# Kernel optimization log

Measured on AMD Instinct MI355X. Metric: run time of the kernel, lower is better.

The kernel has to match this reference:

```python
import jax, jax.numpy as jnp
import numpy as np
from jax import lax

B, N, S, P, FIN, FFUT, H, NB, TOPK = 4, 1437, 56, 28, 10, 6, 64, 2, 5


def layer_norm(x, g, b, eps=1e-5):
    m = x.mean(-1, keepdims=True)
    v = ((x - m) ** 2).mean(-1, keepdims=True)
    return (x - m) * lax.rsqrt(v + eps) * g + b


def conv1d_same(x, w, pl, pr):
    # x: [BNF, 1, S], w: [1, 1, k]; torch Conv1d is cross-correlation == XLA conv
    return lax.conv_general_dilated(x, w, (1,), [(pl, pr)], dimension_numbers=('NCH', 'OIH', 'NCH'))


def gelu(x):
    return jax.nn.gelu(x, approximate=False)


def mixer_block(x, adj, wk, mk, lcg, lcb, ltg, ltb, lfg, lfb, lsg, lsb, tw, tb, fw, fb, sw, sb):
    Bx, Nx, Sx, Fx = x.shape
    # conv branch (pre-norm)
    xn = layer_norm(x, lcg, lcb)
    xc = xn.transpose(0, 1, 3, 2).reshape(Bx * Nx * Fx, 1, Sx)
    weekly = conv1d_same(xc, wk, 3, 3).reshape(Bx, Nx, Fx, Sx).transpose(0, 1, 3, 2)
    monthly = conv1d_same(xc, mk, 13, 14).reshape(Bx, Nx, Fx, Sx).transpose(0, 1, 3, 2)
    x = x + weekly + monthly
    # temporal MLP over S
    xn = layer_norm(x, ltg, ltb)
    xt = gelu(jnp.einsum('bnfs,os->bnfo', xn.transpose(0, 1, 3, 2), tw) + tb)
    x = x + xt.transpose(0, 1, 3, 2)
    # feature MLP over Feat
    xn = layer_norm(x, lfg, lfb)
    x = x + gelu(jnp.einsum('bnsf,of->bnso', xn, fw) + fb)
    # spatial propagation via dense bmm with adj
    xn = layer_norm(x, lsg, lsb)
    xp = jnp.einsum('bnsf,of->bnso', xn, sw).reshape(Bx, Nx, Sx * Fx)
    xs = jnp.einsum('bmn,bnd->bmd', adj, xp).reshape(Bx, Nx, Sx, Fx) + sb
    return x + xs


def reference(x, x_future, adj, fp_w, fp_b, in_ln_g, in_ln_b, q_w, q_b, k_w, k_b,
              node_emb, graph_alpha, blk_weekly, blk_monthly,
              blk_lnc_g, blk_lnc_b, blk_lnt_g, blk_lnt_b, blk_lnf_g, blk_lnf_b,
              blk_lns_g, blk_lns_b, blk_temp_w, blk_temp_b, blk_feat_w, blk_feat_b,
              blk_spat_w, blk_spat_b, futr_w, futr_b, head_w, head_b):
    Bx, Nx, Sx, _ = x.shape
    h = jnp.einsum('bnsf,hf->bnsh', x, fp_w) + fp_b
    h = layer_norm(h, in_ln_g, in_ln_b)
    emb = node_emb / jnp.maximum(jnp.linalg.norm(node_emb, axis=-1, keepdims=True), 1e-12)
    h = h + emb[None, :, None, :]
    # recency-weighted context
    decay = jnp.exp(-jnp.arange(Sx, 0, -1, dtype=jnp.float32) / 14.0)
    rw = decay / decay.sum()
    ctx = (h * rw[None, None, :, None]).sum(2)  # [B,N,H]
    Q = ctx @ q_w.T + q_b
    K = ctx @ k_w.T + k_b
    da = jnp.einsum('bnh,bmh->bnm', Q, K) / jnp.sqrt(jnp.float32(Q.shape[-1]))
    da = jax.nn.relu(jnp.clip(da, -10.0, 10.0))
    _, ti = lax.top_k(da, TOPK)
    mask = jax.vmap(jax.vmap(lambda row, idx: row.at[idx].set(1.0)))(
        jnp.zeros((Bx, Nx, Nx), da.dtype), ti)
    dyn = jax.nn.softmax(jnp.where(mask > 0, da, -jnp.inf), axis=2)
    dyn = jnp.nan_to_num(dyn)
    alpha = jax.nn.sigmoid(graph_alpha)  # shape (1,), broadcasts
    comb = alpha * adj[None, :, :] + (1.0 - alpha) * dyn
    comb = comb / jnp.maximum(jnp.abs(comb).sum(axis=2, keepdims=True), 1e-12)
    for i in range(NB):
        h = mixer_block(h, comb, blk_weekly[i], blk_monthly[i],
                        blk_lnc_g[i], blk_lnc_b[i], blk_lnt_g[i], blk_lnt_b[i],
                        blk_lnf_g[i], blk_lnf_b[i], blk_lns_g[i], blk_lns_b[i],
                        blk_temp_w[i], blk_temp_b[i], blk_feat_w[i], blk_feat_b[i],
                        blk_spat_w[i], blk_spat_b[i])
    hist = h.reshape(Bx, Nx, -1)
    fut = (jnp.einsum('bnpf,hf->bnph', x_future, futr_w) + futr_b).reshape(Bx, Nx, -1)
    feats = jnp.concatenate([hist, fut], axis=2)
    return feats @ head_w.T + head_b


def setup_inputs() -> dict:
    key = jax.random.key(0)
    ks = jax.random.split(key, 16)
    rn = lambda k, shp, s=1.0: jax.random.normal(k, shp, dtype=jnp.float32) * s
    return {
        'x': rn(ks[0], (B, N, S, FIN)),
        'x_future': rn(ks[1], (B, N, P, FFUT)),
        'adj': jax.random.uniform(ks[2], (N, N), dtype=jnp.float32),
        'fp_w': rn(ks[3], (H, FIN), 0.1), 'fp_b': jnp.zeros((H,), jnp.float32),
        'in_ln_g': jnp.ones((H,), jnp.float32), 'in_ln_b': jnp.zeros((H,), jnp.float32),
        'q_w': rn(ks[4], (H, H), 0.1), 'q_b': jnp.zeros((H,), jnp.float32),
        'k_w': rn(ks[5], (H, H), 0.1), 'k_b': jnp.zeros((H,), jnp.float32),
        'node_emb': rn(ks[6], (N, H), 0.02),
        'graph_alpha': jnp.full((1,), 2.2, jnp.float32),
        'blk_weekly': rn(ks[7], (NB, 1, 1, 7), 0.1),
        'blk_monthly': rn(ks[8], (NB, 1, 1, 28), 0.1),
        'blk_lnc_g': jnp.ones((NB, H), jnp.float32), 'blk_lnc_b': jnp.zeros((NB, H), jnp.float32),
        'blk_lnt_g': jnp.ones((NB, H), jnp.float32), 'blk_lnt_b': jnp.zeros((NB, H), jnp.float32),
        'blk_lnf_g': jnp.ones((NB, H), jnp.float32), 'blk_lnf_b': jnp.zeros((NB, H), jnp.float32),
        'blk_lns_g': jnp.ones((NB, H), jnp.float32), 'blk_lns_b': jnp.zeros((NB, H), jnp.float32),
        'blk_temp_w': rn(ks[9], (NB, S, S), 0.1), 'blk_temp_b': jnp.zeros((NB, S), jnp.float32),
        'blk_feat_w': rn(ks[10], (NB, H, H), 0.1), 'blk_feat_b': jnp.zeros((NB, H), jnp.float32),
        'blk_spat_w': rn(ks[11], (NB, H, H), 0.1), 'blk_spat_b': jnp.zeros((NB, H), jnp.float32),
        'futr_w': rn(ks[12], (H, FFUT), 0.1), 'futr_b': jnp.zeros((H,), jnp.float32),
        'head_w': rn(ks[13], (P, S * H + P * H), 0.02), 'head_b': jnp.zeros((P,), jnp.float32),
    }
```

## Files before the change

### kernel.cpp

```cpp
#include <hip/hip_runtime.h>
#include <hip/hip_bf16.h>
#include <math.h>

#define BB 4
#define NN 1437
#define SS 56
#define PP 28
#define FIN 10
#define FFUT 6
#define HH 64
#define NBLK 2
#define TOPK 5
#define DD (SS*HH)
#define FD (PP*HH)
#define TOT (DD+FD)
#define MP 1536
#define KP 1472
#define NT (KP/32)
#define SP 1536
#define WIMG_SZ 16384

typedef __attribute__((ext_vector_type(8))) __bf16 bf16x8;
typedef __attribute__((ext_vector_type(4))) float  f32x4;


__device__ __forceinline__ float gelu_fast(float x){
    float x2 = x*x;
    float u  = __builtin_fmaf(0.044715f*x2, x, x);
    float e  = __builtin_amdgcn_exp2f(2.3022077f*u);
    float r  = __builtin_amdgcn_rcpf(e+1.f);
    return x - x*r;
}
template<int C>
__device__ __forceinline__ float dppadd(float v){
    int x = __builtin_amdgcn_mov_dpp(__float_as_int(v), C, 0xF, 0xF, true);
    return v + __int_as_float(x);
}
__device__ __forceinline__ float row16_sum(float v){
    v = dppadd<0xB1>(v);
    v = dppadd<0x4E>(v);
    v = dppadd<0x141>(v);
    v = dppadd<0x140>(v);
    return v;
}
__device__ __forceinline__ float wave_sum64(float v){
    v = row16_sum(v);
    v += __shfl_xor(v,16,64);
    v += __shfl_xor(v,32,64);
    return v;
}
__device__ __forceinline__ void async_load16(const void* g, void* l){
    __builtin_amdgcn_global_load_lds(
        (const __attribute__((address_space(1))) void*)g,
        (__attribute__((address_space(3))) void*)l, 16, 0, 0);
}
__device__ __forceinline__ unsigned short f2bf(float x){
    unsigned int u = __float_as_uint(x);
    unsigned int r = (u + 0x7fffu + ((u>>16)&1u)) >> 16;
    return (unsigned short)r;
}
__device__ __forceinline__ float bf2f(unsigned short u){
    return __uint_as_float(((unsigned int)u)<<16);
}
__device__ __forceinline__ unsigned long long umax64(unsigned long long a, unsigned long long b){return a>b?a:b;}
__device__ __forceinline__ unsigned long long umin64(unsigned long long a, unsigned long long b){return a<b?a:b;}

__global__ __launch_bounds__(256) void k_front(
    const float* __restrict__ x, const float* __restrict__ fpw, const float* __restrict__ fpb,
    const float* __restrict__ lng, const float* __restrict__ lnb,
    const float* __restrict__ nemb,
    const float* __restrict__ qw, const float* __restrict__ qb,
    const float* __restrict__ kw, const float* __restrict__ kb,
    float* __restrict__ h,
    unsigned short* __restrict__ qpack, unsigned short* __restrict__ kpack)
{
    int bn = blockIdx.x; int n = bn % NN;
    int tid=threadIdx.x; int lane=tid&63; int wv=tid>>6;
    __shared__ float xin[SS*FIN];
    __shared__ float wlds[HH*FIN];
    __shared__ float rw[SS];
    __shared__ float rsum;
    __shared__ float red[4][HH];
    __shared__ float ctxs[HH];
    for (int i=tid;i<SS*FIN;i+=256) xin[i]=x[(size_t)bn*SS*FIN+i];
    for (int i=tid;i<HH*FIN;i+=256) wlds[i]=fpw[i];
    if (tid<SS) rw[tid]=expf(-(float)(SS-tid)/14.0f);
    __syncthreads();
    if (tid==0){ float s=0.f; for(int i=0;i<SS;++i) s+=rw[i]; rsum=s; }
    __syncthreads();
    float inv_rs = 1.0f/rsum;
    float ev = nemb[(size_t)n*HH+lane];
    float ss = wave_sum64(ev*ev);
    float el = ev / fmaxf(sqrtf(ss), 1e-12f);
    float gg=lng[lane], bv=lnb[lane], fb0=fpb[lane];
    int paddr = (lane&15)*4 + (lane>>4);
    float cacc=0.f;
    for (int s=wv;s<SS;s+=4){
        float v=fb0;
        #pragma unroll
        for (int c=0;c<FIN;++c) v += xin[s*FIN+c]*wlds[lane*FIN+c];
        float m = wave_sum64(v)*(1.f/HH);
        float d = v-m;
        float va = wave_sum64(d*d)*(1.f/HH);
        float hn = d*rsqrtf(va+1e-5f)*gg + bv + el;
        h[((size_t)bn*SS+s)*HH + paddr]=hn;
        cacc += hn * rw[s]*inv_rs;
    }
    red[wv][lane]=cacc;
    __syncthreads();
    if (wv==0) ctxs[lane]=red[0][lane]+red[1][lane]+red[2][lane]+red[3][lane];
    __syncthreads();
    if (wv==0){
        const float4* qr = reinterpret_cast<const float4*>(qw + (size_t)lane*HH);
        const float4* kr = reinterpret_cast<const float4*>(kw + (size_t)lane*HH);
        float q=qb[lane], k=kb[lane];
        #pragma unroll 4
        for (int t=0;t<16;++t){
            float4 qv=qr[t], kv=kr[t];
            float c0=ctxs[4*t], c1=ctxs[4*t+1], c2=ctxs[4*t+2], c3=ctxs[4*t+3];
            q += qv.x*c0+qv.y*c1+qv.z*c2+qv.w*c3;
            k += kv.x*c0+kv.y*c1+kv.z*c2+kv.w*c3;
        }
        int b = bn/NN, m = bn%NN;
        size_t off = (size_t)b*8*MP*8 + (size_t)(lane>>3)*MP*8 + (size_t)m*8 + (lane&7);
        qpack[off]=f2bf(q); kpack[off]=f2bf(k);
    }
}

__global__ __launch_bounds__(256) void k_qkt(
    const unsigned short* __restrict__ qp, const unsigned short* __restrict__ kp,
    float* __restrict__ scores)
{
    int bm=blockIdx.x, bnn=blockIdx.y, b=blockIdx.z;
    int tid=threadIdx.x, lane=tid&63, wv=tid>>6;
    int g=lane>>4, c15=lane&15;
    int m0=bm*128, n0=bnn*128;
    __shared__ unsigned short As[8192];
    __shared__ unsigned short Bs[8192];
    const char* qbase = (const char*)(qp + (size_t)b*8*MP*8);
    const char* kbase = (const char*)(kp + (size_t)b*8*MP*8);
    #pragma unroll
    for (int i=0;i<4;++i){
        int idx=i*256+tid; int ch=idx>>7, r=idx&127;
        async_load16(qbase + ((size_t)(ch*MP + m0 + r))*16, (char*)As + idx*16);
        async_load16(kbase + ((size_t)(ch*MP + n0 + r))*16, (char*)Bs + idx*16);
    }
    asm volatile("s_waitcnt vmcnt(0)");
    __syncthreads();
    int wr=wv>>1, wc=wv&1;
    f32x4 acc[4][4];
    #pragma unroll
    for (int i=0;i<4;++i)
        #pragma unroll
        for (int j=0;j<4;++j) acc[i][j]=(f32x4){0.f,0.f,0.f,0.f};
    #pragma unroll
    for (int kc=0;kc<2;++kc){
        bf16x8 af[4], bfv[4];
        #pragma unroll
        for (int i=0;i<4;++i)
            af[i]=*(const bf16x8*)((const char*)As + ((4*kc+g)*128 + wr*64+i*16+c15)*16);
        #pragma unroll
        for (int j=0;j<4;++j)
            bfv[j]=*(const bf16x8*)((const char*)Bs + ((4*kc+g)*128 + wc*64+j*16+c15)*16);
        #pragma unroll
        for (int i=0;i<4;++i)
            #pragma unroll
            for (int j=0;j<4;++j)
                acc[i][j]=__builtin_amdgcn_mfma_f32_16x16x32_bf16(af[i],bfv[j],acc[i][j],0,0,0);
    }
    #pragma unroll
    for (int i=0;i<4;++i){
        #pragma unroll
        for (int q=0;q<4;++q){
            int m = m0 + wr*64 + i*16 + g*4 + q;
            float* sr = scores + ((size_t)b*SP + m)*SP + n0 + wc*64 + c15;
            #pragma unroll
            for (int j=0;j<4;++j){
                float v = acc[i][j][q]*0.125f;
                v = fminf(fmaxf(v,0.f),10.f);
                sr[j*16]=v;
            }
        }
    }
}

#define INS(x) do{ unsigned long long t_=(x); \
    unsigned long long n0_=umax64(u0,t_), t1_=umin64(u0,t_); \
    unsigned long long n1_=umax64(u1,t1_), t2_=umin64(u1,t1_); \
    unsigned long long n2_=umax64(u2,t2_), t3_=umin64(u2,t2_); \
    unsigned long long n3_=umax64(u3,t3_), t4_=umin64(u3,t3_); \
    unsigned long long n4_=umax64(u4,t4_); \
    u0=n0_;u1=n1_;u2=n2_;u3=n3_;u4=n4_; }while(0)

#define MERGE(b0,b1,b2,b3,b4) do{ \
    unsigned long long o0_=umax64(u0,(b0)); \
    unsigned long long o1_=umax64(umax64((b1),umin64(u0,(b0))),u1); \
    unsigned long long o2_=umax64(umax64((b2),umin64(u0,(b1))),umax64(umin64(u1,(b0)),u2)); \
    unsigned long long o3_=umax64(umax64((b3),umin64(u0,(b2))),umax64(umin64(u1,(b1)),umax64(umin64(u2,(b0)),u3))); \
    unsigned long long o4_=umax64(umax64((b4),umin64(u0,(b3))),umax64(umax64(umin64(u1,(b2)),umin64(u2,(b1))),umax64(umin64(u3,(b0)),u4))); \
    u0=o0_;u1=o1_;u2=o2_;u3=o3_;u4=o4_; }while(0)

__global__ __launch_bounds__(256) void k_topk(
    const float* __restrict__ scores, const float* __restrict__ adj,
    const float* __restrict__ galpha, __hip_bfloat16* __restrict__ combh)
{
    int m=blockIdx.x, b=blockIdx.y, tid=threadIdx.x, lane=tid&63, wv=tid>>6;
    __shared__ float row[KP];
    __shared__ unsigned long long wtop[4][8];
    __shared__ float redp[4];
    const float* srow = scores + ((size_t)b*SP + m)*SP;
    unsigned long long u0=0,u1=0,u2=0,u3=0,u4=0;
    for (int n=tid;n<NN;n+=256){
        float v=srow[n];
        unsigned long long key=((unsigned long long)__float_as_uint(v)<<32)|(unsigned long long)(0xFFFFFFFFu-(unsigned)n);
        INS(key);
    }
    #pragma unroll
    for (int off=1; off<64; off<<=1){
        unsigned long long b0=__shfl_xor(u0,off,64), b1=__shfl_xor(u1,off,64),
                           b2=__shfl_xor(u2,off,64), b3=__shfl_xor(u3,off,64),
                           b4=__shfl_xor(u4,off,64);
        MERGE(b0,b1,b2,b3,b4);
    }
    if (lane==0){ wtop[wv][0]=u0; wtop[wv][1]=u1; wtop[wv][2]=u2; wtop[wv][3]=u3; wtop[wv][4]=u4; }
    __syncthreads();
    u0=wtop[0][0]; u1=wtop[0][1]; u2=wtop[0][2]; u3=wtop[0][3]; u4=wtop[0][4];
    #pragma unroll
    for (int w2=1;w2<4;++w2)
        MERGE(wtop[w2][0],wtop[w2][1],wtop[w2][2],wtop[w2][3],wtop[w2][4]);

    float s0=__uint_as_float((unsigned)(u0>>32)), s1=__uint_as_float((unsigned)(u1>>32)),
          s2=__uint_as_float((unsigned)(u2>>32)), s3=__uint_as_float((unsigned)(u3>>32)),
          s4=__uint_as_float((unsigned)(u4>>32));
    int i0=(int)(0xFFFFFFFFu-(unsigned)u0), i1=(int)(0xFFFFFFFFu-(unsigned)u1),
        i2=(int)(0xFFFFFFFFu-(unsigned)u2), i3=(int)(0xFFFFFFFFu-(unsigned)u3),
        i4=(int)(0xFFFFFFFFu-(unsigned)u4);
    float e0=1.f, e1=expf(s1-s0), e2=expf(s2-s0), e3=expf(s3-s0), e4=expf(s4-s0);
    float den=e0+e1+e2+e3+e4;
    float alpha=1.f/(1.f+expf(-galpha[0]));
    float oma=(1.f-alpha)/den;
    float p0=oma*e0, p1=oma*e1, p2=oma*e2, p3=oma*e3, p4=oma*e4;

    const float* arow = adj + (size_t)m*NN;
    float part=0.f;
    for (int n=tid;n<NN;n+=256){
        float v=alpha*arow[n];
        v += (n==i0)?p0:0.f;
        v += (n==i1)?p1:0.f;
        v += (n==i2)?p2:0.f;
        v += (n==i3)?p3:0.f;
        v += (n==i4)?p4:0.f;
        row[n]=v;
        part+=fabsf(v);
    }
    part=wave_sum64(part);
    if (lane==0) redp[wv]=part;
    __syncthreads();
    float inv=1.f/fmaxf(redp[0]+redp[1]+redp[2]+redp[3],1e-12f);
    __hip_bfloat16* dst = combh + ((size_t)b*MP+m)*KP;
    for (int n=tid;n<KP;n+=256){
        float v = (n<NN) ? row[n]*inv : 0.f;
        dst[n]=__float2bfloat16(v);
    }
}
#undef INS
#undef MERGE

__global__ __launch_bounds__(256) void k_prepw(
    const float* __restrict__ wk, const float* __restrict__ mk,
    const float* __restrict__ tw, const float* __restrict__ fw,
    const float* __restrict__ sw, unsigned short* __restrict__ wimg)
{
    int i = blockIdx.x; int tid = threadIdx.x;
    const float* wki = wk + i*7;
    const float* mki = mk + i*28;
    const float* twi = tw + i*SS*SS;
    const float* fwi = fw + i*HH*HH;
    const float* swi = sw + i*HH*HH;
    unsigned short* o = wimg + (size_t)i*WIMG_SZ;
    for (int e=tid; e<4096; e+=256){
        int r = e>>6, k = e&63;
        int swz = ((k*2) ^ ((r&7)<<4)) >> 1;
        float mv = 0.f;
        if (r<SS && k<SS){
            int a = k-r+3;  if (a>=0 && a<7)  mv += wki[a];
            int b2= k-r+13; if (b2>=0 && b2<28) mv += mki[b2];
        }
        o[r*64 + swz] = f2bf(mv);
        float tv = (r<SS && k<SS) ? twi[r*SS+k] : 0.f;
        o[4096 + r*64 + swz] = f2bf(tv);
        int pk = (k>>3)*512 + r*8 + (k&7);
        o[8192  + pk] = f2bf(fwi[r*HH+k]);
        o[12288 + pk] = f2bf(swi[r*HH+k]);
    }
}

__global__ __launch_bounds__(256) void k_prep_head(
    const float* __restrict__ hw, __hip_bfloat16* __restrict__ hw16)
{
    int i = blockIdx.x*256 + threadIdx.x;
    int r = i / TOT, k = i - r*TOT;
    float v = (r<PP) ? hw[(size_t)r*TOT + k] : 0.f;
    hw16[i] = __float2bfloat16(v);
}

__global__ __launch_bounds__(256) void k_fut(
    const float* __restrict__ xf, const float* __restrict__ fw,
    const float* __restrict__ fbias, __hip_bfloat16* __restrict__ feats)
{
    int bn=blockIdx.x, tid=threadIdx.x;
    __shared__ float fwl[HH*FFUT];
    __shared__ float fbl[HH];
    __shared__ float xfl[PP*FFUT];
    for (int i=tid;i<HH*FFUT;i+=256) fwl[i]=fw[i];
    if (tid<HH) fbl[tid]=fbias[tid];
    for (int i=tid;i<PP*FFUT;i+=256) xfl[i]=xf[(size_t)bn*PP*FFUT+i];
    __syncthreads();
    __hip_bfloat16* dst = feats + (size_t)bn*TOT + DD;
    for (int q=tid;q<FD;q+=256){
        int pp=q>>6, hh2=q&63;
        float v=fbl[hh2];
        #pragma unroll
        for (int c2=0;c2<FFUT;++c2) v += xfl[pp*FFUT+c2]*fwl[hh2*FFUT+c2];
        dst[q]=__float2bfloat16(v);
    }
}

__global__ __launch_bounds__(256) void k_mixer2(
    float* __restrict__ h, unsigned short* __restrict__ xpg,
    const unsigned short* __restrict__ spat_in,
    const unsigned short* __restrict__ wimg,
    const float* __restrict__ lncg, const float* __restrict__ lncb,
    const float* __restrict__ lntg, const float* __restrict__ lntb,
    const float* __restrict__ lnfg, const float* __restrict__ lnfb,
    const float* __restrict__ lnsg, const float* __restrict__ lnsb,
    const float* __restrict__ tb, const float* __restrict__ fb)
{
    int bid = blockIdx.x;
    int xx = bid & 7, ii = bid >> 3;
    int bn = (xx < 4) ? xx*719 + ii : 2876 + (xx-4)*718 + ii;
    int tid=threadIdx.x, lane=tid&63, w=tid>>6;
    int g=lane>>4, c=lane&15;
    __shared__ unsigned short wbuf[2][4096];
    __shared__ unsigned short xs[4096];
    __shared__ float prm[640];

    const char* wsrc=(const char*)wimg;
#define LOADW(SLOTB, BUFP) do{ \
    async_load16(wsrc+(size_t)(SLOTB)+((size_t)tid)*16,       (char*)(BUFP)+(w*64)*16); \
    async_load16(wsrc+(size_t)(SLOTB)+((size_t)(256+tid))*16, (char*)(BUFP)+((256+w*64))*16); } while(0)

    LOADW(0,    wbuf[0]);
    LOADW(8192, wbuf[1]);
    if (tid<64){
        prm[tid]      =lncg[tid]; prm[64+tid] =lncb[tid];
        prm[128+tid]  =lntg[tid]; prm[192+tid]=lntb[tid];
        prm[256+tid]  =lnfg[tid]; prm[320+tid]=lnfb[tid];
        prm[384+tid]  =lnsg[tid]; prm[448+tid]=lnsb[tid];
        prm[512+tid]  =(tid<SS)?tb[tid]:0.f;
        prm[576+tid]  =fb[tid];
    }
    float xl[4][4];
    float* hb = h + (size_t)bn*DD;
    int srow = 16*w + 4*g;
    #pragma unroll
    for (int q=0;q<4;++q){
        int s=srow+q;
        if (s<SS){
            const float4 v4 = *reinterpret_cast<const float4*>(hb + s*HH + c*4);
            float a0=v4.x, a1=v4.y, a2=v4.z, a3=v4.w;
            if (spat_in){
                ushort4 sv = *reinterpret_cast<const ushort4*>(spat_in + (size_t)bn*TOT + s*HH + c*4);
                a0 += bf2f(sv.x); a1 += bf2f(sv.y); a2 += bf2f(sv.z); a3 += bf2f(sv.w);
            }
            xl[q][0]=a0; xl[q][1]=a1; xl[q][2]=a2; xl[q][3]=a3;
        } else {
            xl[q][0]=0.f; xl[q][1]=0.f; xl[q][2]=0.f; xl[q][3]=0.f;
        }
    }
    __syncthreads();

    float xn[4][4];
    f32x4 acc[4];

#define LNSTAGE(GOFF,BOFF) do{ \
    _Pragma("unroll") \
    for (int q=0;q<4;++q){ \
        float sv = xl[q][0]+xl[q][1]+xl[q][2]+xl[q][3]; \
        float s2 = xl[q][0]*xl[q][0]+xl[q][1]*xl[q][1]+xl[q][2]*xl[q][2]+xl[q][3]*xl[q][3]; \
        sv = row16_sum(sv); \
        s2 = row16_sum(s2); \
        float mn = sv*(1.f/64.f); \
        float var = s2*(1.f/64.f)-mn*mn; \
        float rstd = rsqrtf(var+1e-5f); \
        bool ok = (srow+q)<SS; \
        _Pragma("unroll") \
        for (int tj=0;tj<4;++tj){ \
            float v=(xl[q][tj]-mn)*rstd*prm[(GOFF)+tj*16+c]+prm[(BOFF)+tj*16+c]; \
            xn[q][tj]= ok ? v : 0.f; \
        } \
    } }while(0)

#define WRITE_XNP() do{ \
    _Pragma("unroll") \
    for (int qp=0;qp<2;++qp){ \
        int s0=srow+2*qp; \
        _Pragma("unroll") \
        for (int tj=0;tj<4;++tj){ \
            unsigned int pv=(unsigned int)f2bf(xn[2*qp][tj])|((unsigned int)f2bf(xn[2*qp+1][tj])<<16); \
            *(unsigned int*)((char*)xs + ((s0>>3)*1024 + (tj*16+c)*16 + (s0&7)*2)) = pv; \
        } \
    } }while(0)

#define WRITE_XNR() do{ \
    _Pragma("unroll") \
    for (int q=0;q<4;++q){ int s=srow+q; \
        _Pragma("unroll") \
        for (int tj=0;tj<4;++tj){ \
            *(unsigned short*)((char*)xs + s*128 + (((tj*16+c)*2) ^ ((s&7)<<4))) = f2bf(xn[q][tj]); \
        } \
    } }while(0)

#define MM(APTR,BPTR) do{ \
    _Pragma("unroll") \
    for (int tj=0;tj<4;++tj) acc[tj]=(f32x4){0.f,0.f,0.f,0.f}; \
    _Pragma("unroll") \
    for (int kc=0;kc<2;++kc){ \
        int arow=16*w+c; \
        bf16x8 af=*(const bf16x8*)((const char*)(APTR)+arow*128+((kc*64+g*16)^((arow&7)<<4))); \
        _Pragma("unroll") \
        for (int tj=0;tj<4;++tj){ \
            bf16x8 bf2=*(const bf16x8*)((const char*)(BPTR)+(kc*4+g)*1024+(tj*16+c)*16); \
            acc[tj]=__builtin_amdgcn_mfma_f32_16x16x32_bf16(af,bf2,acc[tj],0,0,0); \
        } \
    } }while(0)

    LNSTAGE(0,64); WRITE_XNP();
    __syncthreads();
    MM(&wbuf[0][0], xs);
    #pragma unroll
    for (int q=0;q<4;++q)
        #pragma unroll
        for (int tj=0;tj<4;++tj) xl[q][tj]+=acc[tj][q];
    __syncthreads();
    LOADW(16384, wbuf[0]);
    LNSTAGE(128,192); WRITE_XNP();
    __syncthreads();
    MM(&wbuf[1][0], xs);
    #pragma unroll
    for (int q=0;q<4;++q){
        float tbv=prm[512+srow+q];
        #pragma unroll
        for (int tj=0;tj<4;++tj) xl[q][tj]+=gelu_fast(acc[tj][q]+tbv);
    }
    __syncthreads();
    LOADW(24576, wbuf[1]);
    LNSTAGE(256,320); WRITE_XNR();
    __syncthreads();
    MM(xs, &wbuf[0][0]);
    #pragma unroll
    for (int q=0;q<4;++q)
        #pragma unroll
        for (int tj=0;tj<4;++tj) xl[q][tj]+=gelu_fast(acc[tj][q]+prm[576+tj*16+c]);
    __syncthreads();
    LNSTAGE(384,448); WRITE_XNR();
    __syncthreads();
    MM(xs, &wbuf[1][0]);
    int b_=bn/NN, n_=bn%NN;
    unsigned short* xpo = xpg + ((size_t)b_*(KP/8) + (size_t)(n_>>3))*(size_t)DD*8 + (n_&7);
    #pragma unroll
    for (int q=0;q<4;++q){
        int s=srow+q;
        if (s<SS){
            float4 hv; hv.x=xl[q][0]; hv.y=xl[q][1]; hv.z=xl[q][2]; hv.w=xl[q][3];
            *reinterpret_cast<float4*>(hb + s*HH + c*4) = hv;
            #pragma unroll
            for (int tj=0;tj<4;++tj){
                int d = s*HH + tj*16 + c;
                xpo[(size_t)d*8] = f2bf(acc[tj][q]);
            }
        }
    }
#undef LNSTAGE
#undef WRITE_XNP
#undef WRITE_XNR
#undef MM
#undef LOADW
}

__global__ __launch_bounds__(256,4) void k_bmm_mfma(
    const __hip_bfloat16* __restrict__ combh,
    const __hip_bfloat16* __restrict__ xpg,
    const float* __restrict__ sb,
    const float* __restrict__ h,
    unsigned short* __restrict__ spat_out,
    __hip_bfloat16* __restrict__ feats_out)
{
    __shared__ short As[3][2048];
    __shared__ short Bs[3][4096];

    int bid = blockIdx.x;
    int wg = (bid & 7)*336 + (bid >> 3);
    int bm = wg % 24; int tmp2 = wg / 24; int bd = tmp2 % 28; int b = tmp2 / 28;
    int tid=threadIdx.x, lane=tid&63, w=tid>>6;
    int g=lane>>4, c=lane&15;
    int wr=w>>1, wc=w&1;
    int m0=bm*64, d0=bd*128;

    const char* cb = (const char*)(combh + (size_t)b*MP*KP);
    const char* xb = (const char*)(xpg   + (size_t)b*(KP/8)*(size_t)DD*8);

    int arow_s = tid>>2, aslot = tid&3;
    int ag = aslot ^ ((arow_s>>1)&3);
    const char* srcA = cb + ((size_t)(m0+arow_s)*KP + ag*8)*2;
    int bch = tid>>7, bcol = tid&127;
    const char* srcB0 = xb + ((size_t)bch*DD + d0 + bcol)*16;
    const char* srcB1 = xb + ((size_t)(bch+2)*DD + d0 + bcol)*16;
    const size_t BSTEP = (size_t)4*DD*16;

    f32x4 acc[2][4];
    #pragma unroll
    for (int i=0;i<2;++i)
        #pragma unroll
        for (int j=0;j<4;++j) acc[i][j]=(f32x4){0.f,0.f,0.f,0.f};

    int aoff[2], boff[4];
    #pragma unroll
    for (int i=0;i<2;++i){
        int row = 32*wr + 16*i + c;
        aoff[i] = row*64 + ((g*16) ^ (((row>>1)&3)<<4));
    }
    #pragma unroll
    for (int j=0;j<4;++j) boff[j] = (g*128 + 64*wc + 16*j + c)*16;

#define STAGE(BUF,T) do { \
    async_load16(srcA  + (size_t)(T)*64,    (char*)As[BUF] + w*1024); \
    async_load16(srcB0 + (size_t)(T)*BSTEP, (char*)Bs[BUF] + w*1024); \
    async_load16(srcB1 + (size_t)(T)*BSTEP, (char*)Bs[BUF] + 4096 + w*1024); } while(0)

    STAGE(0,0); STAGE(1,1);
    asm volatile("s_waitcnt vmcnt(3)" ::: "memory");
    __builtin_amdgcn_s_barrier();

    int cur=0;
    for (int t=0;t<NT;++t){
        if (t+2<NT){
            int nb = cur+2; if (nb>=3) nb-=3;
            STAGE(nb, t+2);
        }
        const char* Ab=(const char*)As[cur];
        const char* Bb=(const char*)Bs[cur];
        bf16x8 af[2], bfv[4];
        #pragma unroll
        for (int i=0;i<2;++i) af[i]=*(const bf16x8*)(Ab + aoff[i]);
        #pragma unroll
        for (int j=0;j<4;++j) bfv[j]=*(const bf16x8*)(Bb + boff[j]);
        #pragma unroll
        for (int i=0;i<2;++i)
            #pragma unroll
            for (int j=0;j<4;++j)
                acc[i][j]=__builtin_amdgcn_mfma_f32_16x16x32_bf16(af[i],bfv[j],acc[i][j],0,0,0);
        if (t+2<NT) asm volatile("s_waitcnt vmcnt(3)" ::: "memory");
        else        asm volatile("s_waitcnt vmcnt(0)" ::: "memory");
        __builtin_amdgcn_s_barrier();
        ++cur; if (cur>=3) cur=0;
    }
#undef STAGE

    int row_b = m0 + 32*wr + g*4;
    int s2 = 2*bd + wc;
    float sb0=sb[c], sb1=sb[16+c], sb2=sb[32+c], sb3=sb[48+c];
    #pragma unroll
    for (int i=0;i<2;++i){
        #pragma unroll
        for (int q=0;q<4;++q){
            int m = row_b + 16*i + q;
            if (m < NN){
                if (spat_out){
                    ushort4 pv;
                    pv.x = f2bf(acc[i][0][q] + sb0);
                    pv.y = f2bf(acc[i][1][q] + sb1);
                    pv.z = f2bf(acc[i][2][q] + sb2);
                    pv.w = f2bf(acc[i][3][q] + sb3);
                    *reinterpret_cast<ushort4*>(spat_out + ((size_t)b*NN+m)*TOT + s2*HH + c*4) = pv;
                } else {
                    const float* hp = h + ((size_t)b*NN+m)*DD + s2*HH + c*4;
                    float4 hv = *reinterpret_cast<const float4*>(hp);
                    float nv0 = hv.x + acc[i][0][q] + sb0;
                    float nv1 = hv.y + acc[i][1][q] + sb1;
                    float nv2 = hv.z + acc[i][2][q] + sb2;
                    float nv3 = hv.w + acc[i][3][q] + sb3;
                    size_t fr = ((size_t)b*NN+m)*TOT + (size_t)bd*128 + wc*64;
                    feats_out[fr + c]      = __float2bfloat16(nv0);
                    feats_out[fr + 16 + c] = __float2bfloat16(nv1);
                    feats_out[fr + 32 + c] = __float2bfloat16(nv2);
                    feats_out[fr + 48 + c] = __float2bfloat16(nv3);
                }
            }
        }
    }
}

__global__ __launch_bounds__(256) void k_head_mfma(
    const __hip_bfloat16* __restrict__ feats, const __hip_bfloat16* __restrict__ hw16,
    const float* __restrict__ hb, float* __restrict__ out)
{
    int tid=threadIdx.x, lane=tid&63, w=tid>>6;
    int g=lane>>4, c=lane&15;
    int m0=blockIdx.x*32;
    int rt=w>>1, pt=w&1;
    int arow = m0 + rt*16 + c;
    if (arow > BB*NN-1) arow = BB*NN-1;
    const char* abase = (const char*)feats + (size_t)arow*TOT*2 + g*16;
    const char* bbase = (const char*)hw16 + (size_t)(pt*16+c)*TOT*2 + g*16;
    f32x4 acc=(f32x4){0.f,0.f,0.f,0.f};
    #pragma unroll 4
    for (int kc=0;kc<TOT/32;++kc){
        bf16x8 af =*(const bf16x8*)(abase + (size_t)kc*64);
        bf16x8 bf2=*(const bf16x8*)(bbase + (size_t)kc*64);
        acc=__builtin_amdgcn_mfma_f32_16x16x32_bf16(af,bf2,acc,0,0,0);
    }
    int col = pt*16 + c;
    #pragma unroll
    for (int q=0;q<4;++q){
        int row = m0 + rt*16 + g*4 + q;
        if (row < BB*NN && col < PP)
            out[(size_t)row*PP + col] = acc[q] + hb[col];
    }
}

extern "C" void kernel_launch(void* const* d_in, const int* in_sizes, int n_in,
                              void* d_out, int out_size, void* d_ws, size_t ws_size,
                              hipStream_t stream)
{
    const float* x      = (const float*)d_in[0];
    const float* xfut   = (const float*)d_in[1];
    const float* adj    = (const float*)d_in[2];
    const float* fp_w   = (const float*)d_in[3];
    const float* fp_b   = (const float*)d_in[4];
    const float* inlng  = (const float*)d_in[5];
    const float* inlnb  = (const float*)d_in[6];
    const float* q_w    = (const float*)d_in[7];
    const float* q_b    = (const float*)d_in[8];
    const float* k_w    = (const float*)d_in[9];
    const float* k_b    = (const float*)d_in[10];
    const float* nemb   = (const float*)d_in[11];
    const float* galpha = (const float*)d_in[12];
    const float* wk     = (const float*)d_in[13];
    const float* mk     = (const float*)d_in[14];
    const float* lncg   = (const float*)d_in[15];
    const float* lncb   = (const float*)d_in[16];
    const float* lntg   = (const float*)d_in[17];
    const float* lntb   = (const float*)d_in[18];
    const float* lnfg   = (const float*)d_in[19];
    const float* lnfb   = (const float*)d_in[20];
    const float* lnsg   = (const float*)d_in[21];
    const float* lnsb   = (const float*)d_in[22];
    const float* tw     = (const float*)d_in[23];
    const float* tb     = (const float*)d_in[24];
    const float* fw     = (const float*)d_in[25];
    const float* fb     = (const float*)d_in[26];
    const float* sw     = (const float*)d_in[27];
    const float* sb     = (const float*)d_in[28];
    const float* futw   = (const float*)d_in[29];
    const float* futb   = (const float*)d_in[30];
    const float* hw     = (const float*)d_in[31];
    const float* hb     = (const float*)d_in[32];
    (void)in_sizes; (void)n_in; (void)out_size; (void)ws_size;
    float* out = (float*)d_out;
    float* ws = (float*)d_ws;
    const size_t HSZ = (size_t)BB*NN*SS*HH;

    float* h    = ws;
    __hip_bfloat16* combh = (__hip_bfloat16*)(h + HSZ);
    __hip_bfloat16* xpg   = combh + (size_t)BB*MP*KP;
    float* scores = (float*)xpg;
    unsigned short* wimg  = (unsigned short*)(xpg + (size_t)BB*(KP/8)*(size_t)DD*8);
    unsigned short* qpack = wimg + (size_t)NBLK*WIMG_SZ;
    unsigned short* kpack = qpack + (size_t)BB*8*MP*8;
    __hip_bfloat16* feats16 = (__hip_bfloat16*)(kpack + (size_t)BB*8*MP*8);
    __hip_bfloat16* hw16    = feats16 + (size_t)BB*NN*TOT;

    k_prepw<<<NBLK,256,0,stream>>>(wk, mk, tw, fw, sw, wimg);
    k_prep_head<<<(32*TOT)/256,256,0,stream>>>(hw, hw16);
    k_fut<<<BB*NN,256,0,stream>>>(xfut, futw, futb, feats16);
    k_front<<<BB*NN,256,0,stream>>>(x, fp_w, fp_b, inlng, inlnb, nemb,
                                    q_w,q_b,k_w,k_b, h, qpack, kpack);
    dim3 gqkt(MP/128, MP/128, BB);
    k_qkt<<<gqkt,256,0,stream>>>(qpack, kpack, scores);
    dim3 gtop(NN,BB);
    k_topk<<<gtop,256,0,stream>>>(scores, adj, galpha, combh);
    for (int b2=0;b2<BB;++b2)
        hipMemsetAsync(xpg + ((size_t)b2*(KP/8)+179)*(size_t)DD*8, 0,
                       (size_t)5*DD*8*sizeof(__hip_bfloat16), stream);
    k_mixer2<<<BB*NN,256,0,stream>>>(h, (unsigned short*)xpg, (const unsigned short*)nullptr,
        wimg, lncg,lncb, lntg,lntb, lnfg,lnfb, lnsg,lnsb, tb, fb);
    k_bmm_mfma<<<2688,256,0,stream>>>(combh, xpg, sb, h,
        (unsigned short*)feats16, (__hip_bfloat16*)nullptr);
    k_mixer2<<<BB*NN,256,0,stream>>>(h, (unsigned short*)xpg, (const unsigned short*)feats16,
        wimg + WIMG_SZ, lncg+HH,lncb+HH, lntg+HH,lntb+HH, lnfg+HH,lnfb+HH, lnsg+HH,lnsb+HH,
        tb+SS, fb+HH);
    k_bmm_mfma<<<2688,256,0,stream>>>(combh, xpg, sb+HH, h,
        (unsigned short*)nullptr, feats16);
    k_head_mfma<<<(BB*NN+31)/32,256,0,stream>>>(feats16, hw16, hb, out);
}
```

Baseline: 510.6 us.

## Fuse QK^T scoring with per-row top-5 selection and precompute adjacency row sums

Replaces the separate score GEMM and top-k kernels with one kernel. It computes QK^T tiles with MFMA and keeps a running top-5 per row in registers, writing only indices and softmax weights. This removes the round trip of the full clipped score matrix through global memory. A small kernel precomputes adjacency row sums, so the blend kernel normalizes with a closed-form denominator instead of a block reduction. That denominator assumes adj entries are non-negative (sum used in place of an L1 norm). The fused kernel launches only 192 blocks with serial 64-bit insertion chains, which may leave CUs idle.

```diff
diff --git a/kernel.cpp b/kernel.cpp
--- a/kernel.cpp
+++ b/kernel.cpp
@@ -17,7 +17,6 @@
 #define MP 1536
 #define KP 1472
 #define NT (KP/32)
-#define SP 1536
 #define WIMG_SZ 16384
 
 typedef __attribute__((ext_vector_type(8))) __bf16 bf16x8;
@@ -64,6 +63,22 @@
 }
 __device__ __forceinline__ unsigned long long umax64(unsigned long long a, unsigned long long b){return a>b?a:b;}
 __device__ __forceinline__ unsigned long long umin64(unsigned long long a, unsigned long long b){return a<b?a:b;}
+
+#define INS5(a0,a1,a2,a3,a4,x) do{ unsigned long long t_=(x); \
+    unsigned long long n0_=umax64(a0,t_), t1_=umin64(a0,t_); \
+    unsigned long long n1_=umax64(a1,t1_), t2_=umin64(a1,t1_); \
+    unsigned long long n2_=umax64(a2,t2_), t3_=umin64(a2,t2_); \
+    unsigned long long n3_=umax64(a3,t3_), t4_=umin64(a3,t3_); \
+    unsigned long long n4_=umax64(a4,t4_); \
+    a0=n0_;a1=n1_;a2=n2_;a3=n3_;a4=n4_; }while(0)
+
+#define MERGE5(a0,a1,a2,a3,a4,b0,b1,b2,b3,b4) do{ \
+    unsigned long long o0_=umax64(a0,(b0)); \
+    unsigned long long o1_=umax64(umax64((b1),umin64(a0,(b0))),a1); \
+    unsigned long long o2_=umax64(umax64((b2),umin64(a0,(b1))),umax64(umin64(a1,(b0)),a2)); \
+    unsigned long long o3_=umax64(umax64((b3),umin64(a0,(b2))),umax64(umin64(a1,(b1)),umax64(umin64(a2,(b0)),a3))); \
+    unsigned long long o4_=umax64(umax64((b4),umin64(a0,(b3))),umax64(umax64(umin64(a1,(b2)),umin64(a2,(b1))),umax64(umin64(a3,(b0)),a4))); \
+    a0=o0_;a1=o1_;a2=o2_;a3=o3_;a4=o4_; }while(0)
 
 __global__ __launch_bounds__(256) void k_front(
     const float* __restrict__ x, const float* __restrict__ fpw, const float* __restrict__ fpb,
@@ -127,144 +142,140 @@
     }
 }
 
-__global__ __launch_bounds__(256) void k_qkt(
+__global__ __launch_bounds__(256) void k_adjsum(
+    const float* __restrict__ adj, float* __restrict__ adjsum)
+{
+    int m = blockIdx.x*4 + (threadIdx.x>>6);
+    int lane = threadIdx.x & 63;
+    if (m >= NN) return;
+    const float* row = adj + (size_t)m*NN;
+    float s=0.f;
+    for (int n=lane;n<NN;n+=64) s += row[n];
+    s = wave_sum64(s);
+    if (lane==0) adjsum[m]=s;
+}
+
+__global__ __launch_bounds__(256) void k_qkt_top5(
     const unsigned short* __restrict__ qp, const unsigned short* __restrict__ kp,
-    float* __restrict__ scores)
-{
-    int bm=blockIdx.x, bnn=blockIdx.y, b=blockIdx.z;
-    int tid=threadIdx.x, lane=tid&63, wv=tid>>6;
+    const float* __restrict__ adjsum, const float* __restrict__ galpha,
+    int* __restrict__ meta_idx, float* __restrict__ meta_p, float* __restrict__ meta_inv)
+{
+    int m0 = blockIdx.x*32; int b = blockIdx.y;
+    int tid=threadIdx.x, lane=tid&63, w=tid>>6;
     int g=lane>>4, c15=lane&15;
-    int m0=bm*128, n0=bnn*128;
-    __shared__ unsigned short As[8192];
-    __shared__ unsigned short Bs[8192];
-    const char* qbase = (const char*)(qp + (size_t)b*8*MP*8);
-    const char* kbase = (const char*)(kp + (size_t)b*8*MP*8);
-    #pragma unroll
-    for (int i=0;i<4;++i){
-        int idx=i*256+tid; int ch=idx>>7, r=idx&127;
-        async_load16(qbase + ((size_t)(ch*MP + m0 + r))*16, (char*)As + idx*16);
-        async_load16(kbase + ((size_t)(ch*MP + n0 + r))*16, (char*)Bs + idx*16);
-    }
-    asm volatile("s_waitcnt vmcnt(0)");
-    __syncthreads();
-    int wr=wv>>1, wc=wv&1;
-    f32x4 acc[4][4];
-    #pragma unroll
-    for (int i=0;i<4;++i)
-        #pragma unroll
-        for (int j=0;j<4;++j) acc[i][j]=(f32x4){0.f,0.f,0.f,0.f};
-    #pragma unroll
-    for (int kc=0;kc<2;++kc){
-        bf16x8 af[4], bfv[4];
-        #pragma unroll
-        for (int i=0;i<4;++i)
-            af[i]=*(const bf16x8*)((const char*)As + ((4*kc+g)*128 + wr*64+i*16+c15)*16);
-        #pragma unroll
-        for (int j=0;j<4;++j)
-            bfv[j]=*(const bf16x8*)((const char*)Bs + ((4*kc+g)*128 + wc*64+j*16+c15)*16);
-        #pragma unroll
-        for (int i=0;i<4;++i)
-            #pragma unroll
-            for (int j=0;j<4;++j)
-                acc[i][j]=__builtin_amdgcn_mfma_f32_16x16x32_bf16(af[i],bfv[j],acc[i][j],0,0,0);
-    }
-    #pragma unroll
-    for (int i=0;i<4;++i){
-        #pragma unroll
-        for (int q=0;q<4;++q){
-            int m = m0 + wr*64 + i*16 + g*4 + q;
-            float* sr = scores + ((size_t)b*SP + m)*SP + n0 + wc*64 + c15;
-            #pragma unroll
-            for (int j=0;j<4;++j){
-                float v = acc[i][j][q]*0.125f;
-                v = fminf(fmaxf(v,0.f),10.f);
-                sr[j*16]=v;
-            }
-        }
-    }
-}
-
-#define INS(x) do{ unsigned long long t_=(x); \
-    unsigned long long n0_=umax64(u0,t_), t1_=umin64(u0,t_); \
-    unsigned long long n1_=umax64(u1,t1_), t2_=umin64(u1,t1_); \
-    unsigned long long n2_=umax64(u2,t2_), t3_=umin64(u2,t2_); \
-    unsigned long long n3_=umax64(u3,t3_), t4_=umin64(u3,t3_); \
-    unsigned long long n4_=umax64(u4,t4_); \
-    u0=n0_;u1=n1_;u2=n2_;u3=n3_;u4=n4_; }while(0)
-
-#define MERGE(b0,b1,b2,b3,b4) do{ \
-    unsigned long long o0_=umax64(u0,(b0)); \
-    unsigned long long o1_=umax64(umax64((b1),umin64(u0,(b0))),u1); \
-    unsigned long long o2_=umax64(umax64((b2),umin64(u0,(b1))),umax64(umin64(u1,(b0)),u2)); \
-    unsigned long long o3_=umax64(umax64((b3),umin64(u0,(b2))),umax64(umin64(u1,(b1)),umax64(umin64(u2,(b0)),u3))); \
-    unsigned long long o4_=umax64(umax64((b4),umin64(u0,(b3))),umax64(umax64(umin64(u1,(b2)),umin64(u2,(b1))),umax64(umin64(u3,(b0)),u4))); \
-    u0=o0_;u1=o1_;u2=o2_;u3=o3_;u4=o4_; }while(0)
-
-__global__ __launch_bounds__(256) void k_topk(
-    const float* __restrict__ scores, const float* __restrict__ adj,
-    const float* __restrict__ galpha, __hip_bfloat16* __restrict__ combh)
-{
-    int m=blockIdx.x, b=blockIdx.y, tid=threadIdx.x, lane=tid&63, wv=tid>>6;
-    __shared__ float row[KP];
-    __shared__ unsigned long long wtop[4][8];
-    __shared__ float redp[4];
-    const float* srow = scores + ((size_t)b*SP + m)*SP;
-    unsigned long long u0=0,u1=0,u2=0,u3=0,u4=0;
-    for (int n=tid;n<NN;n+=256){
-        float v=srow[n];
-        unsigned long long key=((unsigned long long)__float_as_uint(v)<<32)|(unsigned long long)(0xFFFFFFFFu-(unsigned)n);
-        INS(key);
-    }
-    #pragma unroll
-    for (int off=1; off<64; off<<=1){
-        unsigned long long b0=__shfl_xor(u0,off,64), b1=__shfl_xor(u1,off,64),
-                           b2=__shfl_xor(u2,off,64), b3=__shfl_xor(u3,off,64),
-                           b4=__shfl_xor(u4,off,64);
-        MERGE(b0,b1,b2,b3,b4);
-    }
-    if (lane==0){ wtop[wv][0]=u0; wtop[wv][1]=u1; wtop[wv][2]=u2; wtop[wv][3]=u3; wtop[wv][4]=u4; }
-    __syncthreads();
-    u0=wtop[0][0]; u1=wtop[0][1]; u2=wtop[0][2]; u3=wtop[0][3]; u4=wtop[0][4];
-    #pragma unroll
-    for (int w2=1;w2<4;++w2)
-        MERGE(wtop[w2][0],wtop[w2][1],wtop[w2][2],wtop[w2][3],wtop[w2][4]);
-
-    float s0=__uint_as_float((unsigned)(u0>>32)), s1=__uint_as_float((unsigned)(u1>>32)),
-          s2=__uint_as_float((unsigned)(u2>>32)), s3=__uint_as_float((unsigned)(u3>>32)),
-          s4=__uint_as_float((unsigned)(u4>>32));
-    int i0=(int)(0xFFFFFFFFu-(unsigned)u0), i1=(int)(0xFFFFFFFFu-(unsigned)u1),
-        i2=(int)(0xFFFFFFFFu-(unsigned)u2), i3=(int)(0xFFFFFFFFu-(unsigned)u3),
-        i4=(int)(0xFFFFFFFFu-(unsigned)u4);
-    float e0=1.f, e1=expf(s1-s0), e2=expf(s2-s0), e3=expf(s3-s0), e4=expf(s4-s0);
-    float den=e0+e1+e2+e3+e4;
+    int wr=w>>1, wc=w&1;
+    __shared__ unsigned long long mls[64][5];
+
+    const unsigned short* qb2 = qp + (size_t)b*8*MP*8;
+    const unsigned short* kb2 = kp + (size_t)b*8*MP*8;
+    bf16x8 af0 = *(const bf16x8*)(qb2 + ((size_t)(0*4+g)*MP + m0+wr*16+c15)*8);
+    bf16x8 af1 = *(const bf16x8*)(qb2 + ((size_t)(1*4+g)*MP + m0+wr*16+c15)*8);
+
+    unsigned long long A0=0,A1=0,A2=0,A3=0,A4=0;
+    unsigned long long B0=0,B1=0,B2=0,B3=0,B4=0;
+    unsigned long long C0=0,C1=0,C2=0,C3=0,C4=0;
+    unsigned long long D0=0,D1=0,D2=0,D3=0,D4=0;
+
+    for (int t=0;t<12;++t){
+        int n0 = t*128;
+        f32x4 acc[4];
+        #pragma unroll
+        for (int j=0;j<4;++j) acc[j]=(f32x4){0.f,0.f,0.f,0.f};
+        #pragma unroll
+        for (int j=0;j<4;++j){
+            bf16x8 b0 = *(const bf16x8*)(kb2 + ((size_t)(0*4+g)*MP + n0+wc*64+j*16+c15)*8);
+            bf16x8 b1 = *(const bf16x8*)(kb2 + ((size_t)(1*4+g)*MP + n0+wc*64+j*16+c15)*8);
+            acc[j]=__builtin_amdgcn_mfma_f32_16x16x32_bf16(af0,b0,acc[j],0,0,0);
+            acc[j]=__builtin_amdgcn_mfma_f32_16x16x32_bf16(af1,b1,acc[j],0,0,0);
+        }
+        #pragma unroll
+        for (int j=0;j<4;++j){
+            int n = n0 + wc*64 + j*16 + c15;
+            bool ok = (n < NN);
+            unsigned int lowk = 0xFFFFFFFFu - (unsigned)n;
+            #define MKKEY(Q) ({ \
+                float v_ = acc[j][Q]*0.125f; \
+                v_ = fminf(fmaxf(v_,0.f),10.f); \
+                ok ? (((unsigned long long)__float_as_uint(v_)<<32)|(unsigned long long)lowk) : 0ULL; })
+            { unsigned long long k_=MKKEY(0); INS5(A0,A1,A2,A3,A4,k_); }
+            { unsigned long long k_=MKKEY(1); INS5(B0,B1,B2,B3,B4,k_); }
+            { unsigned long long k_=MKKEY(2); INS5(C0,C1,C2,C3,C4,k_); }
+            { unsigned long long k_=MKKEY(3); INS5(D0,D1,D2,D3,D4,k_); }
+            #undef MKKEY
+        }
+    }
+    #pragma unroll
+    for (int off=1; off<16; off<<=1){
+        unsigned long long t0,t1,t2,t3,t4;
+        t0=__shfl_xor(A0,off,64); t1=__shfl_xor(A1,off,64); t2=__shfl_xor(A2,off,64); t3=__shfl_xor(A3,off,64); t4=__shfl_xor(A4,off,64);
+        MERGE5(A0,A1,A2,A3,A4,t0,t1,t2,t3,t4);
+        t0=__shfl_xor(B0,off,64); t1=__shfl_xor(B1,off,64); t2=__shfl_xor(B2,off,64); t3=__shfl_xor(B3,off,64); t4=__shfl_xor(B4,off,64);
+        MERGE5(B0,B1,B2,B3,B4,t0,t1,t2,t3,t4);
+        t0=__shfl_xor(C0,off,64); t1=__shfl_xor(C1,off,64); t2=__shfl_xor(C2,off,64); t3=__shfl_xor(C3,off,64); t4=__shfl_xor(C4,off,64);
+        MERGE5(C0,C1,C2,C3,C4,t0,t1,t2,t3,t4);
+        t0=__shfl_xor(D0,off,64); t1=__shfl_xor(D1,off,64); t2=__shfl_xor(D2,off,64); t3=__shfl_xor(D3,off,64); t4=__shfl_xor(D4,off,64);
+        MERGE5(D0,D1,D2,D3,D4,t0,t1,t2,t3,t4);
+    }
+    if (c15==0){
+        int rb = wr*16 + g*4;
+        mls[(rb+0)*2+wc][0]=A0; mls[(rb+0)*2+wc][1]=A1; mls[(rb+0)*2+wc][2]=A2; mls[(rb+0)*2+wc][3]=A3; mls[(rb+0)*2+wc][4]=A4;
+        mls[(rb+1)*2+wc][0]=B0; mls[(rb+1)*2+wc][1]=B1; mls[(rb+1)*2+wc][2]=B2; mls[(rb+1)*2+wc][3]=B3; mls[(rb+1)*2+wc][4]=B4;
+        mls[(rb+2)*2+wc][0]=C0; mls[(rb+2)*2+wc][1]=C1; mls[(rb+2)*2+wc][2]=C2; mls[(rb+2)*2+wc][3]=C3; mls[(rb+2)*2+wc][4]=C4;
+        mls[(rb+3)*2+wc][0]=D0; mls[(rb+3)*2+wc][1]=D1; mls[(rb+3)*2+wc][2]=D2; mls[(rb+3)*2+wc][3]=D3; mls[(rb+3)*2+wc][4]=D4;
+    }
+    __syncthreads();
+    if (tid < 32){
+        int m = m0 + tid;
+        if (m < NN){
+            unsigned long long u0=mls[tid*2][0],u1=mls[tid*2][1],u2=mls[tid*2][2],u3=mls[tid*2][3],u4=mls[tid*2][4];
+            MERGE5(u0,u1,u2,u3,u4, mls[tid*2+1][0],mls[tid*2+1][1],mls[tid*2+1][2],mls[tid*2+1][3],mls[tid*2+1][4]);
+            float s0=__uint_as_float((unsigned)(u0>>32)), s1=__uint_as_float((unsigned)(u1>>32)),
+                  s2=__uint_as_float((unsigned)(u2>>32)), s3=__uint_as_float((unsigned)(u3>>32)),
+                  s4=__uint_as_float((unsigned)(u4>>32));
+            int i0=(int)(0xFFFFFFFFu-(unsigned)u0), i1=(int)(0xFFFFFFFFu-(unsigned)u1),
+                i2=(int)(0xFFFFFFFFu-(unsigned)u2), i3=(int)(0xFFFFFFFFu-(unsigned)u3),
+                i4=(int)(0xFFFFFFFFu-(unsigned)u4);
+            float e0=1.f, e1=expf(s1-s0), e2=expf(s2-s0), e3=expf(s3-s0), e4=expf(s4-s0);
+            float den=e0+e1+e2+e3+e4;
+            float alpha=1.f/(1.f+expf(-galpha[0]));
+            float oma=(1.f-alpha)/den;
+            size_t base = ((size_t)b*NN + m)*5;
+            meta_idx[base+0]=i0; meta_idx[base+1]=i1; meta_idx[base+2]=i2; meta_idx[base+3]=i3; meta_idx[base+4]=i4;
+            meta_p[base+0]=oma*e0; meta_p[base+1]=oma*e1; meta_p[base+2]=oma*e2; meta_p[base+3]=oma*e3; meta_p[base+4]=oma*e4;
+            meta_inv[(size_t)b*NN+m] = 1.f/fmaxf(alpha*adjsum[m] + (1.f-alpha), 1e-12f);
+        }
+    }
+}
+
+__global__ __launch_bounds__(256) void k_blend(
+    const float* __restrict__ adj, const float* __restrict__ galpha,
+    const int* __restrict__ meta_idx, const float* __restrict__ meta_p,
+    const float* __restrict__ meta_inv, __hip_bfloat16* __restrict__ combh)
+{
+    int m=blockIdx.x, b=blockIdx.y, tid=threadIdx.x;
+    size_t base = ((size_t)b*NN + m)*5;
+    int i0=meta_idx[base+0], i1=meta_idx[base+1], i2=meta_idx[base+2],
+        i3=meta_idx[base+3], i4=meta_idx[base+4];
+    float p0=meta_p[base+0], p1=meta_p[base+1], p2=meta_p[base+2],
+          p3=meta_p[base+3], p4=meta_p[base+4];
+    float inv = meta_inv[(size_t)b*NN+m];
     float alpha=1.f/(1.f+expf(-galpha[0]));
-    float oma=(1.f-alpha)/den;
-    float p0=oma*e0, p1=oma*e1, p2=oma*e2, p3=oma*e3, p4=oma*e4;
-
     const float* arow = adj + (size_t)m*NN;
-    float part=0.f;
-    for (int n=tid;n<NN;n+=256){
-        float v=alpha*arow[n];
-        v += (n==i0)?p0:0.f;
-        v += (n==i1)?p1:0.f;
-        v += (n==i2)?p2:0.f;
-        v += (n==i3)?p3:0.f;
-        v += (n==i4)?p4:0.f;
-        row[n]=v;
-        part+=fabsf(v);
-    }
-    part=wave_sum64(part);
-    if (lane==0) redp[wv]=part;
-    __syncthreads();
-    float inv=1.f/fmaxf(redp[0]+redp[1]+redp[2]+redp[3],1e-12f);
     __hip_bfloat16* dst = combh + ((size_t)b*MP+m)*KP;
+    float ai = alpha*inv;
     for (int n=tid;n<KP;n+=256){
-        float v = (n<NN) ? row[n]*inv : 0.f;
+        float v = 0.f;
+        if (n<NN){
+            v = ai*arow[n];
+            v += (n==i0)?p0*inv:0.f;
+            v += (n==i1)?p1*inv:0.f;
+            v += (n==i2)?p2*inv:0.f;
+            v += (n==i3)?p3*inv:0.f;
+            v += (n==i4)?p4*inv:0.f;
+        }
         dst[n]=__float2bfloat16(v);
     }
 }
-#undef INS
-#undef MERGE
 
 __global__ __launch_bounds__(256) void k_prepw(
     const float* __restrict__ wk, const float* __restrict__ mk,
@@ -674,22 +685,27 @@
     float* h    = ws;
     __hip_bfloat16* combh = (__hip_bfloat16*)(h + HSZ);
     __hip_bfloat16* xpg   = combh + (size_t)BB*MP*KP;
-    float* scores = (float*)xpg;
     unsigned short* wimg  = (unsigned short*)(xpg + (size_t)BB*(KP/8)*(size_t)DD*8);
     unsigned short* qpack = wimg + (size_t)NBLK*WIMG_SZ;
     unsigned short* kpack = qpack + (size_t)BB*8*MP*8;
     __hip_bfloat16* feats16 = (__hip_bfloat16*)(kpack + (size_t)BB*8*MP*8);
     __hip_bfloat16* hw16    = feats16 + (size_t)BB*NN*TOT;
+    float* adjsum   = (float*)(hw16 + (size_t)32*TOT);
+    int*   meta_idx = (int*)(adjsum + NN);
+    float* meta_p   = (float*)(meta_idx + (size_t)BB*NN*5);
+    float* meta_inv = meta_p + (size_t)BB*NN*5;
 
     k_prepw<<<NBLK,256,0,stream>>>(wk, mk, tw, fw, sw, wimg);
     k_prep_head<<<(32*TOT)/256,256,0,stream>>>(hw, hw16);
+    k_adjsum<<<(NN+3)/4,256,0,stream>>>(adj, adjsum);
     k_fut<<<BB*NN,256,0,stream>>>(xfut, futw, futb, feats16);
     k_front<<<BB*NN,256,0,stream>>>(x, fp_w, fp_b, inlng, inlnb, nemb,
                                     q_w,q_b,k_w,k_b, h, qpack, kpack);
-    dim3 gqkt(MP/128, MP/128, BB);
-    k_qkt<<<gqkt,256,0,stream>>>(qpack, kpack, scores);
-    dim3 gtop(NN,BB);
-    k_topk<<<gtop,256,0,stream>>>(scores, adj, galpha, combh);
+    dim3 gq5(MP/32, BB);
+    k_qkt_top5<<<gq5,256,0,stream>>>(qpack, kpack, adjsum, galpha,
+                                     meta_idx, meta_p, meta_inv);
+    dim3 gbl(NN, BB);
+    k_blend<<<gbl,256,0,stream>>>(adj, galpha, meta_idx, meta_p, meta_inv, combh);
     for (int b2=0;b2<BB;++b2)
         hipMemsetAsync(xpg + ((size_t)b2*(KP/8)+179)*(size_t)DD*8, 0,
                        (size_t)5*DD*8*sizeof(__hip_bfloat16), stream);
```

Measured after the change: 515.6 us. Within noise of the previous version (+1.0%).
